# Kernel tuning notes

Measured on AMD Instinct MI355X. Metric: run time of the kernel, lower is better.

Reference implementation:

```python
import jax, jax.numpy as jnp
import numpy as np

N_IN = 100_000
N_OUT = 400_000
K = 27          # 3^3 kernel offsets
C_IN = 64
C_OUT = 32


def setup_inputs() -> dict:
    key = jax.random.key(0)
    k1, k2, k3, k4 = jax.random.split(key, 4)
    feats = jax.random.normal(k1, (N_IN, C_IN), dtype=jnp.float32)
    # Minkowski-style weight: one [C_in, C_out] matrix per kernel offset
    weight = jax.random.normal(k2, (K, C_IN, C_OUT), dtype=jnp.float32) * (1.0 / np.sqrt(C_IN))
    # kernel maps: for each offset, M=N_IN (in_idx, out_idx) pairs
    in_map = jax.random.randint(k3, (K, N_IN), 0, N_IN, dtype=jnp.int64)
    out_map = jax.random.randint(k4, (K, N_IN), 0, N_OUT, dtype=jnp.int64)
    return {"feats": feats, "weight": weight, "in_map": in_map,
            "out_map": out_map, "n_out": N_OUT}


def reference(feats, weight, in_map, out_map, n_out):
    # gather-GEMM-scatter, vectorized over the K kernel offsets
    gathered = feats[in_map]                          # [K, M, C_in]
    msgs = jnp.einsum('kmc,kcd->kmd', gathered, weight)  # [K, M, C_out]
    out = jnp.zeros((n_out, msgs.shape[-1]), dtype=feats.dtype)
    out = out.at[out_map.reshape(-1)].add(msgs.reshape(-1, msgs.shape[-1]))
    return out
```

## Files before the change

### kernel.cpp

```cpp
#include <hip/hip_runtime.h>
#include <hip/hip_bf16.h>
#include <hip/hip_fp16.h>


using short8  = __attribute__((ext_vector_type(8))) short;
using floatx4 = __attribute__((ext_vector_type(4))) float;

constexpr int KOFF = 27;
constexpr int NIN  = 100000;
constexpr int NOUT = 400000;
constexpr int CIN  = 64;
constexpr int COUT = 32;
constexpr int MSGS = NIN;
constexpr int TILES = MSGS / 16;
constexpr int WPB   = 4;

constexpr size_t ACC_BYTES   = (size_t)NOUT * COUT * 2;
constexpr size_t FEATS_BYTES = (size_t)NIN * CIN * 2;

__device__ __forceinline__ short f2bf(float f) {
    union { float f; unsigned u; } v; v.f = f;
    unsigned r = v.u + 0x7fff + ((v.u >> 16) & 1u);
    return (short)(r >> 16);
}

template<bool BF16F>
__global__ __launch_bounds__(256) void spconv_fp16acc_kernel(
    const float*  __restrict__ feats_f32,
    const ushort* __restrict__ feats_bf,
    const float*  __restrict__ weight,
    const int*    __restrict__ in_map,
    const int*    __restrict__ out_map,
    __half2*      __restrict__ accum)
{
    const int k    = blockIdx.y;
    const int wave = threadIdx.x >> 6;
    const int lane = threadIdx.x & 63;
    const int col  = lane & 15;
    const int quad = lane >> 4;

    const int tile = blockIdx.x * WPB + wave;
    if (tile >= TILES) return;
    const int m0 = tile * 16;
    const long long mapbase = (long long)k * MSGS;

    const int in_row = in_map[mapbase + m0 + col];
    int orow[4];
    #pragma unroll
    for (int i = 0; i < 4; ++i) orow[i] = out_map[mapbase + m0 + quad * 4 + i];

    const float* Wk = weight + k * (CIN * COUT);
    short8 bfr[2][2];
    #pragma unroll
    for (int s = 0; s < 2; ++s)
        #pragma unroll
        for (int t = 0; t < 2; ++t)
            #pragma unroll
            for (int j = 0; j < 8; ++j)
                bfr[s][t][j] = f2bf(Wk[(s * 32 + quad * 8 + j) * COUT + 2 * col + t]);

    short8 a0, a1;
    if (BF16F) {
        const ushort* ar = feats_bf + (long long)in_row * CIN;
        a0 = *(const short8*)(ar + quad * 8);
        a1 = *(const short8*)(ar + 32 + quad * 8);
    } else {
        const float* ar = feats_f32 + (long long)in_row * CIN + quad * 8;
        const float4* p0 = (const float4*)ar;
        const float4* p1 = (const float4*)(ar + 32);
        float4 l0 = p0[0], h0 = p0[1], l1 = p1[0], h1 = p1[1];
        a0[0]=f2bf(l0.x); a0[1]=f2bf(l0.y); a0[2]=f2bf(l0.z); a0[3]=f2bf(l0.w);
        a0[4]=f2bf(h0.x); a0[5]=f2bf(h0.y); a0[6]=f2bf(h0.z); a0[7]=f2bf(h0.w);
        a1[0]=f2bf(l1.x); a1[1]=f2bf(l1.y); a1[2]=f2bf(l1.z); a1[3]=f2bf(l1.w);
        a1[4]=f2bf(h1.x); a1[5]=f2bf(h1.y); a1[6]=f2bf(h1.z); a1[7]=f2bf(h1.w);
    }

    floatx4 acc0 = {0.f, 0.f, 0.f, 0.f};
    floatx4 acc1 = {0.f, 0.f, 0.f, 0.f};
    acc0 = __builtin_amdgcn_mfma_f32_16x16x32_bf16(a0, bfr[0][0], acc0, 0, 0, 0);
    acc1 = __builtin_amdgcn_mfma_f32_16x16x32_bf16(a0, bfr[0][1], acc1, 0, 0, 0);
    acc0 = __builtin_amdgcn_mfma_f32_16x16x32_bf16(a1, bfr[1][0], acc0, 0, 0, 0);
    acc1 = __builtin_amdgcn_mfma_f32_16x16x32_bf16(a1, bfr[1][1], acc1, 0, 0, 0);

    #pragma unroll
    for (int i = 0; i < 4; ++i) {
        __half2 h = __floats2half2_rn(acc0[i], acc1[i]);
        unsafeAtomicAdd(accum + (long long)orow[i] * 16 + col, h);
    }
}

__global__ __launch_bounds__(256) void spconv_f32atomic_kernel(
    const float* __restrict__ feats,
    const float* __restrict__ weight,
    const int*   __restrict__ in_map,
    const int*   __restrict__ out_map,
    float*       __restrict__ out)
{
    const int k    = blockIdx.y;
    const int wave = threadIdx.x >> 6;
    const int lane = threadIdx.x & 63;
    const int col  = lane & 15;
    const int quad = lane >> 4;
    const int tile = blockIdx.x * WPB + wave;
    if (tile >= TILES) return;
    const int m0 = tile * 16;
    const long long mapbase = (long long)k * MSGS;

    const float* Wk = weight + k * (CIN * COUT);
    short8 bfr[2][2];
    #pragma unroll
    for (int s = 0; s < 2; ++s)
        #pragma unroll
        for (int t = 0; t < 2; ++t)
            #pragma unroll
            for (int j = 0; j < 8; ++j)
                bfr[s][t][j] = f2bf(Wk[(s * 32 + quad * 8 + j) * COUT + t * 16 + col]);

    const int in_row = in_map[mapbase + m0 + col];
    const float* arow = feats + (long long)in_row * CIN + quad * 8;

    floatx4 acc0 = {0.f, 0.f, 0.f, 0.f};
    floatx4 acc1 = {0.f, 0.f, 0.f, 0.f};
    #pragma unroll
    for (int s = 0; s < 2; ++s) {
        const float4* p = (const float4*)(arow + s * 32);
        float4 lo = p[0], hi = p[1];
        short8 a;
        a[0]=f2bf(lo.x); a[1]=f2bf(lo.y); a[2]=f2bf(lo.z); a[3]=f2bf(lo.w);
        a[4]=f2bf(hi.x); a[5]=f2bf(hi.y); a[6]=f2bf(hi.z); a[7]=f2bf(hi.w);
        acc0 = __builtin_amdgcn_mfma_f32_16x16x32_bf16(a, bfr[s][0], acc0, 0, 0, 0);
        acc1 = __builtin_amdgcn_mfma_f32_16x16x32_bf16(a, bfr[s][1], acc1, 0, 0, 0);
    }
    #pragma unroll
    for (int i = 0; i < 4; ++i) {
        const int orow = out_map[mapbase + m0 + quad * 4 + i];
        float* po = out + (long long)orow * COUT;
        atomicAdd(po + col,      acc0[i]);
        atomicAdd(po + col + 16, acc1[i]);
    }
}

__global__ __launch_bounds__(256) void feats_to_bf16_kernel(
    const float* __restrict__ f, ushort* __restrict__ b)
{
    const int t = blockIdx.x * blockDim.x + threadIdx.x;
    const float4* p = (const float4*)(f + (size_t)t * 8);
    float4 lo = p[0], hi = p[1];
    short8 v;
    v[0]=f2bf(lo.x); v[1]=f2bf(lo.y); v[2]=f2bf(lo.z); v[3]=f2bf(lo.w);
    v[4]=f2bf(hi.x); v[5]=f2bf(hi.y); v[6]=f2bf(hi.z); v[7]=f2bf(hi.w);
    *(short8*)(b + (size_t)t * 8) = v;
}

__global__ __launch_bounds__(256) void h2_to_f32_kernel(
    const __half2* __restrict__ acc, float* __restrict__ out)
{
    const int t = blockIdx.x * blockDim.x + threadIdx.x;
    const __half2* p = acc + (size_t)t * 4;
    float2 f0 = __half22float2(p[0]);
    float2 f1 = __half22float2(p[1]);
    float2 f2 = __half22float2(p[2]);
    float2 f3 = __half22float2(p[3]);
    float4* o = (float4*)out + (size_t)t * 2;
    o[0] = make_float4(f0.x, f0.y, f1.x, f1.y);
    o[1] = make_float4(f2.x, f2.y, f3.x, f3.y);
}

extern "C" void kernel_launch(void* const* d_in, const int* in_sizes, int n_in,
                              void* d_out, int out_size, void* d_ws, size_t ws_size,
                              hipStream_t stream) {
    const float* feats   = (const float*)d_in[0];
    const float* weight  = (const float*)d_in[1];
    const int*   in_map  = (const int*)d_in[2];
    const int*   out_map = (const int*)d_in[3];
    float*       out     = (float*)d_out;

    dim3 grid((TILES + WPB - 1) / WPB, KOFF);
    dim3 block(WPB * 64);

    if (ws_size >= ACC_BYTES + FEATS_BYTES) {
        __half2* accum    = (__half2*)d_ws;
        ushort*  feats_bf = (ushort*)((char*)d_ws + ACC_BYTES);
        hipMemsetAsync(accum, 0, ACC_BYTES, stream);
        feats_to_bf16_kernel<<<(NIN * CIN / 8) / 256, 256, 0, stream>>>(feats, feats_bf);
        spconv_fp16acc_kernel<true><<<grid, block, 0, stream>>>(
            feats, feats_bf, weight, in_map, out_map, accum);
        h2_to_f32_kernel<<<(NOUT * 16 / 4) / 256, 256, 0, stream>>>(accum, out);
    } else if (ws_size >= ACC_BYTES) {
        __half2* accum = (__half2*)d_ws;
        hipMemsetAsync(accum, 0, ACC_BYTES, stream);
        spconv_fp16acc_kernel<false><<<grid, block, 0, stream>>>(
            feats, nullptr, weight, in_map, out_map, accum);
        h2_to_f32_kernel<<<(NOUT * 16 / 4) / 256, 256, 0, stream>>>(accum, out);
    } else {
        hipMemsetAsync(d_out, 0, (size_t)out_size * sizeof(float), stream);
        spconv_f32atomic_kernel<<<grid, block, 0, stream>>>(
            feats, weight, in_map, out_map, out);
    }
}
```

Measured before the change: 267.6 us.

## Bucket messages by output row range so each XCD's atomics stay in its L2

Adds a pre-pass that groups message indices per kernel offset into 8 buckets by output-row range. The conv kernel then assigns bucket blockIdx.x&7, aiming to line each bucket up with one XCD so that XCD's fp16 atomic scatter targets a slice of the accumulator small enough to stay in its L2. The cost is an extra bucketing kernel, a second level of index indirection, and a smaller looping grid. Entries beyond the fixed capacity are silently dropped.

```diff
diff --git a/kernel.cpp b/kernel.cpp
--- a/kernel.cpp
+++ b/kernel.cpp
@@ -15,13 +15,128 @@
 constexpr int TILES = MSGS / 16;
 constexpr int WPB   = 4;
 
+constexpr int NBUCK = 8;
+constexpr int ROWS_PER_BUCK = NOUT / NBUCK;
+constexpr int CAP = 18432;
+constexpr int BLOCKS_PER_BUCK = 8;
+
 constexpr size_t ACC_BYTES   = (size_t)NOUT * COUT * 2;
 constexpr size_t FEATS_BYTES = (size_t)NIN * CIN * 2;
+constexpr size_t LIST_BYTES  = (size_t)KOFF * NBUCK * CAP * 4;
+constexpr size_t CNT_BYTES   = 1024;
 
 __device__ __forceinline__ short f2bf(float f) {
     union { float f; unsigned u; } v; v.f = f;
     unsigned r = v.u + 0x7fff + ((v.u >> 16) & 1u);
     return (short)(r >> 16);
+}
+
+__global__ __launch_bounds__(256) void bucket_kernel(
+    const int* __restrict__ out_map,
+    int* __restrict__ lists,
+    int* __restrict__ gcount)
+{
+    const int k    = blockIdx.y;
+    const int tid  = threadIdx.x;
+    const int mbase = blockIdx.x * 512;
+
+    __shared__ int lbin[NBUCK];
+    __shared__ int gbase[NBUCK];
+    if (tid < NBUCK) lbin[tid] = 0;
+    __syncthreads();
+
+    int mm[2], bk[2], lpos[2], valid[2];
+    #pragma unroll
+    for (int j = 0; j < 2; ++j) {
+        mm[j]    = mbase + j * 256 + tid;
+        valid[j] = mm[j] < MSGS;
+        if (valid[j]) {
+            const int o = out_map[(long long)k * MSGS + mm[j]];
+            bk[j]   = o / ROWS_PER_BUCK;
+            lpos[j] = atomicAdd(&lbin[bk[j]], 1);
+        }
+    }
+    __syncthreads();
+    if (tid < NBUCK) gbase[tid] = atomicAdd(&gcount[k * NBUCK + tid], lbin[tid]);
+    __syncthreads();
+    #pragma unroll
+    for (int j = 0; j < 2; ++j) {
+        if (valid[j]) {
+            const int p = gbase[bk[j]] + lpos[j];
+            if (p < CAP) lists[((long long)(k * NBUCK + bk[j])) * CAP + p] = mm[j];
+        }
+    }
+}
+
+__global__ __launch_bounds__(256) void spconv_bucketed_kernel(
+    const ushort* __restrict__ feats_bf,
+    const float*  __restrict__ weight,
+    const int*    __restrict__ in_map,
+    const int*    __restrict__ out_map,
+    const int*    __restrict__ lists,
+    const int*    __restrict__ gcount,
+    __half2*      __restrict__ accum)
+{
+    const int k    = blockIdx.y;
+    const int b    = blockIdx.x & (NBUCK - 1);
+    const int chnk = blockIdx.x >> 3;
+    const int wave = threadIdx.x >> 6;
+    const int lane = threadIdx.x & 63;
+    const int col  = lane & 15;
+    const int quad = lane >> 4;
+
+    const int count = gcount[k * NBUCK + b];
+    if (count <= 0) return;
+    const int ntiles = (count + 15) >> 4;
+    const int* list = lists + ((long long)(k * NBUCK + b)) * CAP;
+    const long long kM = (long long)k * MSGS;
+
+    const float* Wk = weight + k * (CIN * COUT);
+    short8 bfr[2][2];
+    #pragma unroll
+    for (int s = 0; s < 2; ++s)
+        #pragma unroll
+        for (int t = 0; t < 2; ++t)
+            #pragma unroll
+            for (int j = 0; j < 8; ++j)
+                bfr[s][t][j] = f2bf(Wk[(s * 32 + quad * 8 + j) * COUT + 2 * col + t]);
+
+    const int wstride = BLOCKS_PER_BUCK * WPB;
+    for (int tile = chnk * WPB + wave; tile < ntiles; tile += wstride) {
+        const int base = tile * 16;
+
+        int ecol = base + col;
+        const bool vc = ecol < count;
+        if (!vc) ecol = count - 1;
+        const int mcol   = list[ecol];
+        const int in_row = in_map[kM + mcol];
+
+        const ushort* ar = feats_bf + (long long)in_row * CIN;
+        short8 a0 = *(const short8*)(ar + quad * 8);
+        short8 a1 = *(const short8*)(ar + 32 + quad * 8);
+        if (!vc) { a0 = (short8)0; a1 = (short8)0; }
+
+        int orow[4];
+        #pragma unroll
+        for (int i = 0; i < 4; ++i) {
+            int e = base + quad * 4 + i;
+            if (e >= count) e = count - 1;
+            orow[i] = out_map[kM + list[e]];
+        }
+
+        floatx4 acc0 = {0.f, 0.f, 0.f, 0.f};
+        floatx4 acc1 = {0.f, 0.f, 0.f, 0.f};
+        acc0 = __builtin_amdgcn_mfma_f32_16x16x32_bf16(a0, bfr[0][0], acc0, 0, 0, 0);
+        acc1 = __builtin_amdgcn_mfma_f32_16x16x32_bf16(a0, bfr[0][1], acc1, 0, 0, 0);
+        acc0 = __builtin_amdgcn_mfma_f32_16x16x32_bf16(a1, bfr[1][0], acc0, 0, 0, 0);
+        acc1 = __builtin_amdgcn_mfma_f32_16x16x32_bf16(a1, bfr[1][1], acc1, 0, 0, 0);
+
+        #pragma unroll
+        for (int i = 0; i < 4; ++i) {
+            __half2 h = __floats2half2_rn(acc0[i], acc1[i]);
+            unsafeAtomicAdd(accum + (long long)orow[i] * 16 + col, h);
+        }
+    }
 }
 
 template<bool BF16F>
@@ -38,7 +153,6 @@
     const int lane = threadIdx.x & 63;
     const int col  = lane & 15;
     const int quad = lane >> 4;
-
     const int tile = blockIdx.x * WPB + wave;
     if (tile >= TILES) return;
     const int m0 = tile * 16;
@@ -175,26 +289,37 @@
     const int*   out_map = (const int*)d_in[3];
     float*       out     = (float*)d_out;
 
-    dim3 grid((TILES + WPB - 1) / WPB, KOFF);
-    dim3 block(WPB * 64);
-
-    if (ws_size >= ACC_BYTES + FEATS_BYTES) {
+    if (ws_size >= ACC_BYTES + FEATS_BYTES + LIST_BYTES + CNT_BYTES) {
+        __half2* accum    = (__half2*)d_ws;
+        ushort*  feats_bf = (ushort*)((char*)d_ws + ACC_BYTES);
+        int*     lists    = (int*)((char*)d_ws + ACC_BYTES + FEATS_BYTES);
+        int*     gcount   = (int*)((char*)d_ws + ACC_BYTES + FEATS_BYTES + LIST_BYTES);
+
+        hipMemsetAsync(accum, 0, ACC_BYTES, stream);
+        hipMemsetAsync(gcount, 0, CNT_BYTES, stream);
+        feats_to_bf16_kernel<<<(NIN * CIN / 8) / 256, 256, 0, stream>>>(feats, feats_bf);
+        bucket_kernel<<<dim3((MSGS + 511) / 512, KOFF), 256, 0, stream>>>(
+            out_map, lists, gcount);
+        spconv_bucketed_kernel<<<dim3(NBUCK * BLOCKS_PER_BUCK, KOFF), 256, 0, stream>>>(
+            feats_bf, weight, in_map, out_map, lists, gcount, accum);
+        h2_to_f32_kernel<<<(NOUT * 16 / 4) / 256, 256, 0, stream>>>(accum, out);
+    } else if (ws_size >= ACC_BYTES + FEATS_BYTES) {
         __half2* accum    = (__half2*)d_ws;
         ushort*  feats_bf = (ushort*)((char*)d_ws + ACC_BYTES);
         hipMemsetAsync(accum, 0, ACC_BYTES, stream);
         feats_to_bf16_kernel<<<(NIN * CIN / 8) / 256, 256, 0, stream>>>(feats, feats_bf);
-        spconv_fp16acc_kernel<true><<<grid, block, 0, stream>>>(
+        spconv_fp16acc_kernel<true><<<dim3((TILES + WPB - 1) / WPB, KOFF), 256, 0, stream>>>(
             feats, feats_bf, weight, in_map, out_map, accum);
         h2_to_f32_kernel<<<(NOUT * 16 / 4) / 256, 256, 0, stream>>>(accum, out);
     } else if (ws_size >= ACC_BYTES) {
         __half2* accum = (__half2*)d_ws;
         hipMemsetAsync(accum, 0, ACC_BYTES, stream);
-        spconv_fp16acc_kernel<false><<<grid, block, 0, stream>>>(
+        spconv_fp16acc_kernel<false><<<dim3((TILES + WPB - 1) / WPB, KOFF), 256, 0, stream>>>(
             feats, nullptr, weight, in_map, out_map, accum);
         h2_to_f32_kernel<<<(NOUT * 16 / 4) / 256, 256, 0, stream>>>(accum, out);
     } else {
         hipMemsetAsync(d_out, 0, (size_t)out_size * sizeof(float), stream);
-        spconv_f32atomic_kernel<<<grid, block, 0, stream>>>(
+        spconv_f32atomic_kernel<<<dim3((TILES + WPB - 1) / WPB, KOFF), 256, 0, stream>>>(
             feats, weight, in_map, out_map, out);
     }
 }
```

Measured after the change: 285.0 us. 6.5% more time.

## Use persistent per-offset blocks with software-pipelined map and feature prefetch

Applied to the files above, without the earlier changes.

Replaces the one-tile-per-wave grid with a persistent grid of 64 blocks per kernel offset. Each wave loops over tiles, prefetching index maps two tiles ahead and gathered bf16 features one tile ahead, so gather latency overlaps the MFMA and atomic work. Weight conversion to bf16 is now paid once per wave instead of once per tile. The memset and feature conversion are fused into one prep kernel to save a launch. The catch is that the grid is much smaller (64x27 blocks), so occupancy and latency hiding depend on the prefetch depth and on the atomic throughput.

```diff
diff --git a/kernel.cpp b/kernel.cpp
--- a/kernel.cpp
+++ b/kernel.cpp
@@ -14,9 +14,14 @@
 constexpr int MSGS = NIN;
 constexpr int TILES = MSGS / 16;
 constexpr int WPB   = 4;
+constexpr int BLK_PER_K = 64;
+constexpr int WSTRIDE = BLK_PER_K * WPB;
 
 constexpr size_t ACC_BYTES   = (size_t)NOUT * COUT * 2;
 constexpr size_t FEATS_BYTES = (size_t)NIN * CIN * 2;
+
+constexpr int CVT_BLOCKS  = (NIN * CIN / 8) / 256;
+constexpr int ZERO_BLOCKS = (int)(ACC_BYTES / 16) / 256;
 
 __device__ __forceinline__ short f2bf(float f) {
     union { float f; unsigned u; } v; v.f = f;
@@ -24,9 +29,24 @@
     return (short)(r >> 16);
 }
 
-template<bool BF16F>
-__global__ __launch_bounds__(256) void spconv_fp16acc_kernel(
-    const float*  __restrict__ feats_f32,
+__global__ __launch_bounds__(256) void prep_kernel(
+    const float* __restrict__ f, ushort* __restrict__ b, float4* __restrict__ accz)
+{
+    if (blockIdx.x < CVT_BLOCKS) {
+        const int t = blockIdx.x * 256 + threadIdx.x;
+        const float4* p = (const float4*)(f + (size_t)t * 8);
+        float4 lo = p[0], hi = p[1];
+        short8 v;
+        v[0]=f2bf(lo.x); v[1]=f2bf(lo.y); v[2]=f2bf(lo.z); v[3]=f2bf(lo.w);
+        v[4]=f2bf(hi.x); v[5]=f2bf(hi.y); v[6]=f2bf(hi.z); v[7]=f2bf(hi.w);
+        *(short8*)(b + (size_t)t * 8) = v;
+    } else {
+        const int t = (blockIdx.x - CVT_BLOCKS) * 256 + threadIdx.x;
+        accz[t] = make_float4(0.f, 0.f, 0.f, 0.f);
+    }
+}
+
+__global__ __launch_bounds__(256) void spconv_pipe_kernel(
     const ushort* __restrict__ feats_bf,
     const float*  __restrict__ weight,
     const int*    __restrict__ in_map,
@@ -38,16 +58,7 @@
     const int lane = threadIdx.x & 63;
     const int col  = lane & 15;
     const int quad = lane >> 4;
-
-    const int tile = blockIdx.x * WPB + wave;
-    if (tile >= TILES) return;
-    const int m0 = tile * 16;
-    const long long mapbase = (long long)k * MSGS;
-
-    const int in_row = in_map[mapbase + m0 + col];
-    int orow[4];
-    #pragma unroll
-    for (int i = 0; i < 4; ++i) orow[i] = out_map[mapbase + m0 + quad * 4 + i];
+    const long long kM = (long long)k * MSGS;
 
     const float* Wk = weight + k * (CIN * COUT);
     short8 bfr[2][2];
@@ -59,42 +70,62 @@
             for (int j = 0; j < 8; ++j)
                 bfr[s][t][j] = f2bf(Wk[(s * 32 + quad * 8 + j) * COUT + 2 * col + t]);
 
-    short8 a0, a1;
-    if (BF16F) {
-        const ushort* ar = feats_bf + (long long)in_row * CIN;
-        a0 = *(const short8*)(ar + quad * 8);
-        a1 = *(const short8*)(ar + 32 + quad * 8);
-    } else {
-        const float* ar = feats_f32 + (long long)in_row * CIN + quad * 8;
-        const float4* p0 = (const float4*)ar;
-        const float4* p1 = (const float4*)(ar + 32);
-        float4 l0 = p0[0], h0 = p0[1], l1 = p1[0], h1 = p1[1];
-        a0[0]=f2bf(l0.x); a0[1]=f2bf(l0.y); a0[2]=f2bf(l0.z); a0[3]=f2bf(l0.w);
-        a0[4]=f2bf(h0.x); a0[5]=f2bf(h0.y); a0[6]=f2bf(h0.z); a0[7]=f2bf(h0.w);
-        a1[0]=f2bf(l1.x); a1[1]=f2bf(l1.y); a1[2]=f2bf(l1.z); a1[3]=f2bf(l1.w);
-        a1[4]=f2bf(h1.x); a1[5]=f2bf(h1.y); a1[6]=f2bf(h1.z); a1[7]=f2bf(h1.w);
-    }
-
-    floatx4 acc0 = {0.f, 0.f, 0.f, 0.f};
-    floatx4 acc1 = {0.f, 0.f, 0.f, 0.f};
-    acc0 = __builtin_amdgcn_mfma_f32_16x16x32_bf16(a0, bfr[0][0], acc0, 0, 0, 0);
-    acc1 = __builtin_amdgcn_mfma_f32_16x16x32_bf16(a0, bfr[0][1], acc1, 0, 0, 0);
-    acc0 = __builtin_amdgcn_mfma_f32_16x16x32_bf16(a1, bfr[1][0], acc0, 0, 0, 0);
-    acc1 = __builtin_amdgcn_mfma_f32_16x16x32_bf16(a1, bfr[1][1], acc1, 0, 0, 0);
-
-    #pragma unroll
-    for (int i = 0; i < 4; ++i) {
-        __half2 h = __floats2half2_rn(acc0[i], acc1[i]);
-        unsafeAtomicAdd(accum + (long long)orow[i] * 16 + col, h);
-    }
-}
-
-__global__ __launch_bounds__(256) void spconv_f32atomic_kernel(
-    const float* __restrict__ feats,
-    const float* __restrict__ weight,
-    const int*   __restrict__ in_map,
-    const int*   __restrict__ out_map,
-    float*       __restrict__ out)
+    #define LOAD_MAPS(t, inr, orow)                                   \
+        {                                                             \
+            const int tt = ((t) < TILES) ? (t) : (TILES - 1);         \
+            const long long mb = kM + (long long)tt * 16;             \
+            inr = in_map[mb + col];                                   \
+            _Pragma("unroll")                                         \
+            for (int i = 0; i < 4; ++i) orow[i] = out_map[mb + quad * 4 + i]; \
+        }
+
+    #define LOAD_FEATS(inr, a0, a1)                                   \
+        {                                                             \
+            const ushort* ar = feats_bf + (long long)(inr) * CIN;     \
+            a0 = *(const short8*)(ar + quad * 8);                     \
+            a1 = *(const short8*)(ar + 32 + quad * 8);                \
+        }
+
+    const int t0 = blockIdx.x * WPB + wave;
+
+    int inrA, orowA[4];  LOAD_MAPS(t0,            inrA, orowA);
+    int inrB, orowB[4];  LOAD_MAPS(t0 + WSTRIDE,  inrB, orowB);
+    short8 a0A, a1A;     LOAD_FEATS(inrA, a0A, a1A);
+
+    for (int t = t0; t < TILES; t += WSTRIDE) {
+        int inrC, orowC[4];
+        LOAD_MAPS(t + 2 * WSTRIDE, inrC, orowC);
+        short8 a0B, a1B;
+        LOAD_FEATS(inrB, a0B, a1B);
+
+        floatx4 acc0 = {0.f, 0.f, 0.f, 0.f};
+        floatx4 acc1 = {0.f, 0.f, 0.f, 0.f};
+        acc0 = __builtin_amdgcn_mfma_f32_16x16x32_bf16(a0A, bfr[0][0], acc0, 0, 0, 0);
+        acc1 = __builtin_amdgcn_mfma_f32_16x16x32_bf16(a0A, bfr[0][1], acc1, 0, 0, 0);
+        acc0 = __builtin_amdgcn_mfma_f32_16x16x32_bf16(a1A, bfr[1][0], acc0, 0, 0, 0);
+        acc1 = __builtin_amdgcn_mfma_f32_16x16x32_bf16(a1A, bfr[1][1], acc1, 0, 0, 0);
+
+        #pragma unroll
+        for (int i = 0; i < 4; ++i) {
+            __half2 h = __floats2half2_rn(acc0[i], acc1[i]);
+            unsafeAtomicAdd(accum + (long long)orowA[i] * 16 + col, h);
+        }
+
+        inrA = inrB; a0A = a0B; a1A = a1B;
+        inrB = inrC;
+        #pragma unroll
+        for (int i = 0; i < 4; ++i) { orowA[i] = orowB[i]; orowB[i] = orowC[i]; }
+    }
+    #undef LOAD_MAPS
+    #undef LOAD_FEATS
+}
+
+__global__ __launch_bounds__(256) void spconv_fp16acc_f32feats_kernel(
+    const float*  __restrict__ feats_f32,
+    const float*  __restrict__ weight,
+    const int*    __restrict__ in_map,
+    const int*    __restrict__ out_map,
+    __half2*      __restrict__ accum)
 {
     const int k    = blockIdx.y;
     const int wave = threadIdx.x >> 6;
@@ -106,6 +137,62 @@
     const int m0 = tile * 16;
     const long long mapbase = (long long)k * MSGS;
 
+    const int in_row = in_map[mapbase + m0 + col];
+    int orow[4];
+    #pragma unroll
+    for (int i = 0; i < 4; ++i) orow[i] = out_map[mapbase + m0 + quad * 4 + i];
+
+    const float* Wk = weight + k * (CIN * COUT);
+    short8 bfr[2][2];
+    #pragma unroll
+    for (int s = 0; s < 2; ++s)
+        #pragma unroll
+        for (int t = 0; t < 2; ++t)
+            #pragma unroll
+            for (int j = 0; j < 8; ++j)
+                bfr[s][t][j] = f2bf(Wk[(s * 32 + quad * 8 + j) * COUT + 2 * col + t]);
+
+    const float* ar = feats_f32 + (long long)in_row * CIN + quad * 8;
+    const float4* p0 = (const float4*)ar;
+    const float4* p1 = (const float4*)(ar + 32);
+    float4 l0 = p0[0], h0 = p0[1], l1 = p1[0], h1 = p1[1];
+    short8 a0, a1;
+    a0[0]=f2bf(l0.x); a0[1]=f2bf(l0.y); a0[2]=f2bf(l0.z); a0[3]=f2bf(l0.w);
+    a0[4]=f2bf(h0.x); a0[5]=f2bf(h0.y); a0[6]=f2bf(h0.z); a0[7]=f2bf(h0.w);
+    a1[0]=f2bf(l1.x); a1[1]=f2bf(l1.y); a1[2]=f2bf(l1.z); a1[3]=f2bf(l1.w);
+    a1[4]=f2bf(h1.x); a1[5]=f2bf(h1.y); a1[6]=f2bf(h1.z); a1[7]=f2bf(h1.w);
+
+    floatx4 acc0 = {0.f, 0.f, 0.f, 0.f};
+    floatx4 acc1 = {0.f, 0.f, 0.f, 0.f};
+    acc0 = __builtin_amdgcn_mfma_f32_16x16x32_bf16(a0, bfr[0][0], acc0, 0, 0, 0);
+    acc1 = __builtin_amdgcn_mfma_f32_16x16x32_bf16(a0, bfr[0][1], acc1, 0, 0, 0);
+    acc0 = __builtin_amdgcn_mfma_f32_16x16x32_bf16(a1, bfr[1][0], acc0, 0, 0, 0);
+    acc1 = __builtin_amdgcn_mfma_f32_16x16x32_bf16(a1, bfr[1][1], acc1, 0, 0, 0);
+
+    #pragma unroll
+    for (int i = 0; i < 4; ++i) {
+        __half2 h = __floats2half2_rn(acc0[i], acc1[i]);
+        unsafeAtomicAdd(accum + (long long)orow[i] * 16 + col, h);
+    }
+}
+
+__global__ __launch_bounds__(256) void spconv_f32atomic_kernel(
+    const float* __restrict__ feats,
+    const float* __restrict__ weight,
+    const int*   __restrict__ in_map,
+    const int*   __restrict__ out_map,
+    float*       __restrict__ out)
+{
+    const int k    = blockIdx.y;
+    const int wave = threadIdx.x >> 6;
+    const int lane = threadIdx.x & 63;
+    const int col  = lane & 15;
+    const int quad = lane >> 4;
+    const int tile = blockIdx.x * WPB + wave;
+    if (tile >= TILES) return;
+    const int m0 = tile * 16;
+    const long long mapbase = (long long)k * MSGS;
+
     const float* Wk = weight + k * (CIN * COUT);
     short8 bfr[2][2];
     #pragma unroll
@@ -138,18 +225,6 @@
         atomicAdd(po + col,      acc0[i]);
         atomicAdd(po + col + 16, acc1[i]);
     }
-}
-
-__global__ __launch_bounds__(256) void feats_to_bf16_kernel(
-    const float* __restrict__ f, ushort* __restrict__ b)
-{
-    const int t = blockIdx.x * blockDim.x + threadIdx.x;
-    const float4* p = (const float4*)(f + (size_t)t * 8);
-    float4 lo = p[0], hi = p[1];
-    short8 v;
-    v[0]=f2bf(lo.x); v[1]=f2bf(lo.y); v[2]=f2bf(lo.z); v[3]=f2bf(lo.w);
-    v[4]=f2bf(hi.x); v[5]=f2bf(hi.y); v[6]=f2bf(hi.z); v[7]=f2bf(hi.w);
-    *(short8*)(b + (size_t)t * 8) = v;
 }
 
 __global__ __launch_bounds__(256) void h2_to_f32_kernel(
@@ -175,26 +250,24 @@
     const int*   out_map = (const int*)d_in[3];
     float*       out     = (float*)d_out;
 
-    dim3 grid((TILES + WPB - 1) / WPB, KOFF);
-    dim3 block(WPB * 64);
-
     if (ws_size >= ACC_BYTES + FEATS_BYTES) {
         __half2* accum    = (__half2*)d_ws;
         ushort*  feats_bf = (ushort*)((char*)d_ws + ACC_BYTES);
-        hipMemsetAsync(accum, 0, ACC_BYTES, stream);
-        feats_to_bf16_kernel<<<(NIN * CIN / 8) / 256, 256, 0, stream>>>(feats, feats_bf);
-        spconv_fp16acc_kernel<true><<<grid, block, 0, stream>>>(
-            feats, feats_bf, weight, in_map, out_map, accum);
+
+        prep_kernel<<<CVT_BLOCKS + ZERO_BLOCKS, 256, 0, stream>>>(
+            feats, feats_bf, (float4*)accum);
+        spconv_pipe_kernel<<<dim3(BLK_PER_K, KOFF), 256, 0, stream>>>(
+            feats_bf, weight, in_map, out_map, accum);
         h2_to_f32_kernel<<<(NOUT * 16 / 4) / 256, 256, 0, stream>>>(accum, out);
     } else if (ws_size >= ACC_BYTES) {
         __half2* accum = (__half2*)d_ws;
         hipMemsetAsync(accum, 0, ACC_BYTES, stream);
-        spconv_fp16acc_kernel<false><<<grid, block, 0, stream>>>(
-            feats, nullptr, weight, in_map, out_map, accum);
+        spconv_fp16acc_f32feats_kernel<<<dim3((TILES + WPB - 1) / WPB, KOFF), 256, 0, stream>>>(
+            feats, weight, in_map, out_map, accum);
         h2_to_f32_kernel<<<(NOUT * 16 / 4) / 256, 256, 0, stream>>>(accum, out);
     } else {
         hipMemsetAsync(d_out, 0, (size_t)out_size * sizeof(float), stream);
-        spconv_f32atomic_kernel<<<grid, block, 0, stream>>>(
+        spconv_f32atomic_kernel<<<dim3((TILES + WPB - 1) / WPB, KOFF), 256, 0, stream>>>(
             feats, weight, in_map, out_map, out);
     }
 }
```

After: 260.1 us. -2.8%, faster.
